# Optimization experiments

Measured on AMD Instinct MI355X. Metric: run time of the kernel, lower is better.

Reference implementation:

```python
import jax, jax.numpy as jnp
import numpy as np

N = 20000      # nodes
E = 320000     # edges (before self loops)
D_IN = 256
D_H = 256
D_E = 8
NEG_SLOPE = 0.2


def setup_inputs() -> dict:
    key = jax.random.key(0)
    ks = jax.random.split(key, 12)
    x = jax.random.normal(ks[0], (N, D_IN), jnp.float32)
    edge_index = jax.random.randint(ks[1], (2, E), 0, N, dtype=jnp.int32)
    edge_attr = jax.random.normal(ks[2], (E, D_E), jnp.float32)
    batch = jnp.zeros((N,), jnp.int32)

    def gat_params(k, d_in):
        k1, k2, k3 = jax.random.split(k, 3)
        W = jax.random.normal(k1, (d_in, D_H), jnp.float32) * (1.0 / np.sqrt(d_in))
        a_s = jax.random.normal(k2, (D_H,), jnp.float32) * 0.1
        a_d = jax.random.normal(k3, (D_H,), jnp.float32) * 0.1
        b = jnp.zeros((D_H,), jnp.float32)
        return W, a_s, a_d, b

    W1, as1, ad1, b1 = gat_params(ks[3], D_IN)
    W2, as2, ad2, b2 = gat_params(ks[4], D_H)
    W3, as3, ad3, b3 = gat_params(ks[5], D_H)
    return dict(x=x, edge_index=edge_index, edge_attr=edge_attr, batch=batch,
                W1=W1, as1=as1, ad1=ad1, b1=b1,
                W2=W2, as2=as2, ad2=ad2, b2=b2,
                W3=W3, as3=as3, ad3=ad3, b3=b3)


def gat_conv(x, src, dst, W, a_src, a_dst, b):
    # PyG GATConv, heads=1: h = x W; alpha_e = leakyrelu(<h_src,a_s> + <h_dst,a_d>)
    h = x @ W                                  # [N, D_H]
    s = h @ a_src                              # [N]
    d = h @ a_dst                              # [N]
    alpha = jax.nn.leaky_relu(s[src] + d[dst], NEG_SLOPE)   # [Etot]
    n = h.shape[0]
    m = jax.ops.segment_max(alpha, dst, num_segments=n)     # per-dst max
    ex = jnp.exp(alpha - m[dst])
    denom = jax.ops.segment_sum(ex, dst, num_segments=n)
    w = ex / (denom[dst] + 1e-16)
    out = jax.ops.segment_sum(h[src] * w[:, None], dst, num_segments=n)
    return out + b


def reference(x, edge_index, edge_attr, batch,
              W1, as1, ad1, b1, W2, as2, ad2, b2, W3, as3, ad3, b3):
    # row-normalize input features (zero norms -> 1e-8)
    norms = jnp.linalg.norm(x, axis=1, keepdims=True)
    norms = jnp.where(norms == 0, 1e-8, norms)
    x = x / norms

    # add self loops once (GATConv default add_self_loops=True);
    # edge_attr is ignored since edge_dim=None in GATConv defaults.
    loop = jnp.arange(N, dtype=edge_index.dtype)
    src = jnp.concatenate([edge_index[0], loop])
    dst = jnp.concatenate([edge_index[1], loop])

    x = jax.nn.gelu(gat_conv(x, src, dst, W1, as1, ad1, b1), approximate=False)
    x = jax.nn.gelu(gat_conv(x, src, dst, W2, as2, ad2, b2), approximate=False)
    x = jax.nn.gelu(gat_conv(x, src, dst, W3, as3, ad3, b3), approximate=False)
    return x
```

## Files before the change

kernel.cpp:

```cpp
#include <hip/hip_runtime.h>
#include <math.h>

#define NN 20000
#define EE 320000
#define DD 256
#define ETOT (EE + NN)
#define EDGE_CAP 1536

typedef __attribute__((ext_vector_type(8))) short bf8;
typedef __attribute__((ext_vector_type(4))) float f32x4;

__device__ __forceinline__ float gelu_exact(float x) {
    return 0.5f * x * (1.0f + erff(x * 0.70710678118654752f));
}

__device__ __forceinline__ unsigned short f2bf(float v) {
    unsigned u = __float_as_uint(v);
    u += 0x7fffu + ((u >> 16) & 1u);
    return (unsigned short)(u >> 16);
}
__device__ __forceinline__ float bf2f(unsigned short h) {
    return __uint_as_float(((unsigned)h) << 16);
}
__device__ __forceinline__ void split2(float v, unsigned short& hi, unsigned short& lo) {
    hi = f2bf(v);
    lo = f2bf(v - bf2f(hi));
}

__global__ __launch_bounds__(256) void norm_k(const float* __restrict__ X,
                                              unsigned short* __restrict__ Xh,
                                              unsigned short* __restrict__ Xl,
                                              float* __restrict__ sdZero,
                                              int* __restrict__ deg) {
    int t = threadIdx.x;
    int bid = blockIdx.x;
    if (t < 24) sdZero[bid * 24 + t] = 0.0f;
    if (t >= 32 && t < 36) deg[bid * 4 + (t - 32)] = 1;

    int wave = (bid * 256 + t) >> 6;
    int lane = t & 63;
    const float4 v = *(const float4*)&X[wave * DD + lane * 4];
    float ss = v.x * v.x + v.y * v.y + v.z * v.z + v.w * v.w;
    for (int off = 32; off > 0; off >>= 1) ss += __shfl_down(ss, off, 64);
    ss = __shfl(ss, 0, 64);
    float n = sqrtf(ss);
    if (n == 0.0f) n = 1e-8f;
    float inv = 1.0f / n;
    float o[4] = {v.x * inv, v.y * inv, v.z * inv, v.w * inv};
    ushort4 hv, lv;
    split2(o[0], hv.x, lv.x);
    split2(o[1], hv.y, lv.y);
    split2(o[2], hv.z, lv.z);
    split2(o[3], hv.w, lv.w);
    *(ushort4*)&Xh[wave * DD + lane * 4] = hv;
    *(ushort4*)&Xl[wave * DD + lane * 4] = lv;
}

__global__ __launch_bounds__(256) void splitw_k(const float* __restrict__ W1, const float* __restrict__ W2,
                                                const float* __restrict__ W3, unsigned short* __restrict__ Whl) {
    __shared__ float tile[64][65];
    int t = threadIdx.x;
    int k0 = blockIdx.x * 64;
    int c0 = blockIdx.y * 64;
    int z = blockIdx.z;
    const float* W = (z == 0) ? W1 : (z == 1) ? W2 : W3;
    unsigned short* Wht = Whl + (size_t)z * 2 * DD * DD;
    unsigned short* Wlt = Wht + DD * DD;
#pragma unroll
    for (int i = 0; i < 16; ++i) {
        int idx = t + i * 256;
        int r = idx >> 6, c = idx & 63;
        tile[r][c] = W[(k0 + r) * DD + c0 + c];
    }
    __syncthreads();
#pragma unroll
    for (int i = 0; i < 16; ++i) {
        int idx = t + i * 256;
        int r = idx >> 6, c = idx & 63;
        float v = tile[c][r];
        unsigned short hi, lo;
        split2(v, hi, lo);
        Wht[(c0 + r) * DD + k0 + c] = hi;
        Wlt[(c0 + r) * DD + k0 + c] = lo;
    }
}

__global__ void count_k(const int* __restrict__ ei, int* deg) {
    int e = blockIdx.x * 256 + threadIdx.x;
    if (e < EE) atomicAdd(&deg[ei[EE + e]], 1);
}

#define SCAN_T 1024
#define ITEMS 20
__global__ __launch_bounds__(SCAN_T) void scan_k(const int* __restrict__ deg, int* __restrict__ offs,
                                                 int* __restrict__ cursor, int* __restrict__ csr) {
    __shared__ int part[SCAN_T];
    int t = threadIdx.x;
    int base = t * ITEMS;
    int local[ITEMS];
    int sum = 0;
#pragma unroll
    for (int i = 0; i < ITEMS; ++i) {
        int idx = base + i;
        int v = (idx < NN) ? deg[idx] : 0;
        local[i] = v;
        sum += v;
    }
    part[t] = sum;
    __syncthreads();
    for (int s = 1; s < SCAN_T; s <<= 1) {
        int v = (t >= s) ? part[t - s] : 0;
        __syncthreads();
        part[t] += v;
        __syncthreads();
    }
    int run = (t == 0) ? 0 : part[t - 1];
#pragma unroll
    for (int i = 0; i < ITEMS; ++i) {
        int idx = base + i;
        if (idx < NN) {
            offs[idx] = run;
            cursor[idx] = run + 1;
            csr[run] = idx;
            run += local[i];
        }
    }
    if (t == SCAN_T - 1) offs[NN] = part[SCAN_T - 1];
}

__global__ void fill_k(const int* __restrict__ ei, int* cursor, int* __restrict__ csr) {
    int e = blockIdx.x * 256 + threadIdx.x;
    if (e < EE) {
        int s = ei[e];
        int d = ei[EE + e];
        int p = atomicAdd(&cursor[d], 1);
        csr[p] = s;
    }
}

#define LDB 40
__global__ __launch_bounds__(256) void gemm_sd(const unsigned short* __restrict__ Xh,
                                               const unsigned short* __restrict__ Xl,
                                               const unsigned short* __restrict__ Bh,
                                               const unsigned short* __restrict__ Bl,
                                               const float* __restrict__ a_s,
                                               const float* __restrict__ a_d,
                                               float* __restrict__ H,
                                               float* __restrict__ sArr,
                                               float* __restrict__ dArr) {
    __shared__ unsigned short sBh[128 * LDB], sBl[128 * LDB];
    int t = threadIdx.x;
    int m0 = blockIdx.x * 64;
    int n0 = blockIdx.y * 128;
    int w = t >> 6, l = t & 63;
    int rofs = l & 15, kch = l >> 4;

    f32x4 acc[8] = {};

    int c1 = t, c2 = t + 256;
    int br1 = c1 >> 2, bo1 = (c1 & 3) * 8;
    int br2 = c2 >> 2, bo2 = (c2 & 3) * 8;
    const unsigned short* Bh1 = &Bh[(n0 + br1) * DD + bo1];
    const unsigned short* Bh2 = &Bh[(n0 + br2) * DD + bo2];
    const unsigned short* Bl1 = &Bl[(n0 + br1) * DD + bo1];
    const unsigned short* Bl2 = &Bl[(n0 + br2) * DD + bo2];
    bf8 rbh1 = *(const bf8*)Bh1;
    bf8 rbh2 = *(const bf8*)Bh2;
    bf8 rbl1 = *(const bf8*)Bl1;
    bf8 rbl2 = *(const bf8*)Bl2;

    int arow = m0 + w * 16 + rofs;
    bool aval = arow < NN;
    const unsigned short* Ahp = &Xh[(size_t)arow * DD + kch * 8];
    const unsigned short* Alp = &Xl[(size_t)arow * DD + kch * 8];
    bf8 zero = {0, 0, 0, 0, 0, 0, 0, 0};
    bf8 ah = aval ? *(const bf8*)Ahp : zero;
    bf8 al = aval ? *(const bf8*)Alp : zero;

    for (int k0 = 0; k0 < DD; k0 += 32) {
        if (k0) __syncthreads();
        *(bf8*)&sBh[br1 * LDB + bo1] = rbh1;
        *(bf8*)&sBh[br2 * LDB + bo2] = rbh2;
        *(bf8*)&sBl[br1 * LDB + bo1] = rbl1;
        *(bf8*)&sBl[br2 * LDB + bo2] = rbl2;
        __syncthreads();
        int kn = k0 + 32;
        bf8 nah = zero, nal = zero;
        if (kn < DD) {
            rbh1 = *(const bf8*)(Bh1 + kn);
            rbh2 = *(const bf8*)(Bh2 + kn);
            rbl1 = *(const bf8*)(Bl1 + kn);
            rbl2 = *(const bf8*)(Bl2 + kn);
            if (aval) {
                nah = *(const bf8*)(Ahp + kn);
                nal = *(const bf8*)(Alp + kn);
            }
        }
#pragma unroll
        for (int nt = 0; nt < 8; ++nt) {
            int r = nt * 16 + rofs;
            bf8 bh = *(const bf8*)&sBh[r * LDB + kch * 8];
            bf8 bl = *(const bf8*)&sBl[r * LDB + kch * 8];
            acc[nt] = __builtin_amdgcn_mfma_f32_16x16x32_bf16(ah, bh, acc[nt], 0, 0, 0);
            acc[nt] = __builtin_amdgcn_mfma_f32_16x16x32_bf16(ah, bl, acc[nt], 0, 0, 0);
            acc[nt] = __builtin_amdgcn_mfma_f32_16x16x32_bf16(al, bh, acc[nt], 0, 0, 0);
        }
        ah = nah;
        al = nal;
    }
    int row0 = m0 + w * 16 + (l >> 4) * 4;
    int colb = l & 15;
    float sp[4] = {0, 0, 0, 0}, dp[4] = {0, 0, 0, 0};
#pragma unroll
    for (int nt = 0; nt < 8; ++nt) {
        int cc = n0 + nt * 16 + colb;
        float vas = a_s[cc], vad = a_d[cc];
#pragma unroll
        for (int r = 0; r < 4; ++r) {
            int row = row0 + r;
            if (row < NN) H[(size_t)row * DD + cc] = acc[nt][r];
            sp[r] += acc[nt][r] * vas;
            dp[r] += acc[nt][r] * vad;
        }
    }
#pragma unroll
    for (int m = 1; m < 16; m <<= 1) {
#pragma unroll
        for (int r = 0; r < 4; ++r) {
            sp[r] += __shfl_xor(sp[r], m, 64);
            dp[r] += __shfl_xor(dp[r], m, 64);
        }
    }
    if (colb == 0) {
#pragma unroll
        for (int r = 0; r < 4; ++r) {
            int row = row0 + r;
            if (row < NN) {
                atomicAdd(&sArr[row], sp[r]);
                atomicAdd(&dArr[row], dp[r]);
            }
        }
    }
}

__global__ __launch_bounds__(256) void spmm_k(const float* __restrict__ H, const float* __restrict__ sArr,
                                              const float* __restrict__ dArr, const int* __restrict__ offs,
                                              const int* __restrict__ csr, const float* __restrict__ bias,
                                              unsigned short* __restrict__ Oh,
                                              unsigned short* __restrict__ Ol,
                                              float* __restrict__ outf32) {
    __shared__ float wLds[EDGE_CAP];
    __shared__ int sLds[EDGE_CAP];
    int t = threadIdx.x;
    int sub = t & 7;
    int g = t >> 3;
    int dst0 = blockIdx.y * 32;
    int dst = dst0 + g;
    int dim = blockIdx.x * 32 + sub * 4;

    int blkBeg = offs[dst0];
    int beg = offs[dst], end = offs[dst + 1];
    float dd = dArr[dst];

    float den = 0.0f;
    for (int e = beg + sub; e < end; e += 8) {
        int s = csr[e];
        float a = sArr[s] + dd;
        a = (a > 0.0f) ? a : 0.2f * a;
        float wv = expf(a);
        wLds[e - blkBeg] = wv;
        sLds[e - blkBeg] = s;
        den += wv;
    }
    den += __shfl_xor(den, 1, 64);
    den += __shfl_xor(den, 2, 64);
    den += __shfl_xor(den, 4, 64);
    float inv = 1.0f / den;
    for (int e = beg + sub; e < end; e += 8) wLds[e - blkBeg] *= inv;
    __syncthreads();

    const float* Hs = H + dim;
    float4 A0 = make_float4(0, 0, 0, 0), A1 = A0, A2 = A0, A3 = A0;
    int e = beg - blkBeg, lend = end - blkBeg;
    for (; e + 3 < lend; e += 4) {
        int s0 = sLds[e], s1 = sLds[e + 1], s2 = sLds[e + 2], s3 = sLds[e + 3];
        float w0 = wLds[e], w1 = wLds[e + 1], w2 = wLds[e + 2], w3 = wLds[e + 3];
        const float4 h0 = *(const float4*)&Hs[(size_t)s0 * DD];
        const float4 h1 = *(const float4*)&Hs[(size_t)s1 * DD];
        const float4 h2 = *(const float4*)&Hs[(size_t)s2 * DD];
        const float4 h3 = *(const float4*)&Hs[(size_t)s3 * DD];
        A0.x += w0 * h0.x; A0.y += w0 * h0.y; A0.z += w0 * h0.z; A0.w += w0 * h0.w;
        A1.x += w1 * h1.x; A1.y += w1 * h1.y; A1.z += w1 * h1.z; A1.w += w1 * h1.w;
        A2.x += w2 * h2.x; A2.y += w2 * h2.y; A2.z += w2 * h2.z; A2.w += w2 * h2.w;
        A3.x += w3 * h3.x; A3.y += w3 * h3.y; A3.z += w3 * h3.z; A3.w += w3 * h3.w;
    }
    for (; e < lend; ++e) {
        int s0 = sLds[e];
        float w0 = wLds[e];
        const float4 h0 = *(const float4*)&Hs[(size_t)s0 * DD];
        A0.x += w0 * h0.x; A0.y += w0 * h0.y; A0.z += w0 * h0.z; A0.w += w0 * h0.w;
    }

    const float4 b = *(const float4*)&bias[dim];
    float o0 = gelu_exact(A0.x + A1.x + A2.x + A3.x + b.x);
    float o1 = gelu_exact(A0.y + A1.y + A2.y + A3.y + b.y);
    float o2 = gelu_exact(A0.z + A1.z + A2.z + A3.z + b.z);
    float o3 = gelu_exact(A0.w + A1.w + A2.w + A3.w + b.w);

    ushort4 hv, lv;
    split2(o0, hv.x, lv.x);
    split2(o1, hv.y, lv.y);
    split2(o2, hv.z, lv.z);
    split2(o3, hv.w, lv.w);
    *(ushort4*)&Oh[dst * DD + dim] = hv;
    *(ushort4*)&Ol[dst * DD + dim] = lv;
    if (outf32) {
        float4 o = make_float4(o0, o1, o2, o3);
        *(float4*)&outf32[dst * DD + dim] = o;
    }
}

extern "C" void kernel_launch(void* const* d_in, const int* in_sizes, int n_in,
                              void* d_out, int out_size, void* d_ws, size_t ws_size,
                              hipStream_t stream) {
    const float* x  = (const float*)d_in[0];
    const int* ei   = (const int*)d_in[1];
    const float* W1 = (const float*)d_in[4];
    const float* as1 = (const float*)d_in[5];
    const float* ad1 = (const float*)d_in[6];
    const float* b1 = (const float*)d_in[7];
    const float* W2 = (const float*)d_in[8];
    const float* as2 = (const float*)d_in[9];
    const float* ad2 = (const float*)d_in[10];
    const float* b2 = (const float*)d_in[11];
    const float* W3 = (const float*)d_in[12];
    const float* as3 = (const float*)d_in[13];
    const float* ad3 = (const float*)d_in[14];
    const float* b3 = (const float*)d_in[15];

    float* H = (float*)d_ws;
    unsigned short* Xh = (unsigned short*)(H + (size_t)NN * DD);
    unsigned short* Xl = Xh + (size_t)NN * DD;
    unsigned short* Whl = Xl + (size_t)NN * DD;
    float* sd = (float*)(Whl + (size_t)6 * DD * DD);
    int* offs = (int*)(sd + (size_t)6 * NN);
    int* cursor = offs + (NN + 1);
    int* csr = cursor + NN;
    int* deg = csr + ETOT;

    float* sA1 = sd,           *dA1 = sd + NN;
    float* sA2 = sd + 2 * NN,  *dA2 = sd + 3 * NN;
    float* sA3 = sd + 4 * NN,  *dA3 = sd + 5 * NN;
    unsigned short* Wt1 = Whl;
    unsigned short* Wt2 = Whl + (size_t)2 * DD * DD;
    unsigned short* Wt3 = Whl + (size_t)4 * DD * DD;

    norm_k<<<NN / 4, 256, 0, stream>>>(x, Xh, Xl, sd, deg);
    count_k<<<(EE + 255) / 256, 256, 0, stream>>>(ei, deg);
    scan_k<<<1, SCAN_T, 0, stream>>>(deg, offs, cursor, csr);
    fill_k<<<(EE + 255) / 256, 256, 0, stream>>>(ei, cursor, csr);
    splitw_k<<<dim3(4, 4, 3), 256, 0, stream>>>(W1, W2, W3, Whl);

    dim3 ggrid((NN + 63) / 64, DD / 128);
    dim3 sgrid(DD / 32, NN / 32);

    gemm_sd<<<ggrid, 256, 0, stream>>>(Xh, Xl, Wt1, Wt1 + DD * DD, as1, ad1, H, sA1, dA1);
    spmm_k<<<sgrid, 256, 0, stream>>>(H, sA1, dA1, offs, csr, b1, Xh, Xl, nullptr);
    gemm_sd<<<ggrid, 256, 0, stream>>>(Xh, Xl, Wt2, Wt2 + DD * DD, as2, ad2, H, sA2, dA2);
    spmm_k<<<sgrid, 256, 0, stream>>>(H, sA2, dA2, offs, csr, b2, Xh, Xl, nullptr);
    gemm_sd<<<ggrid, 256, 0, stream>>>(Xh, Xl, Wt3, Wt3 + DD * DD, as3, ad3, H, sA3, dA3);
    spmm_k<<<sgrid, 256, 0, stream>>>(H, sA3, dA3, offs, csr, b3, Xh, Xl, (float*)d_out);
}
```

Before: 337.1 us.

## Precompute edge attention weights once per layer and grid-stride SpMM blocks

Adds a separate alpha_k kernel that computes exp(leakyrelu) edge weights once per edge, using a new per-edge destination array written during CSR construction. Previously each of the 8 dim-column blocks recomputed them. The SpMM kernel now loads weights and source indices with vectorized copies into LDS, folds the normalization into the final scale, and grid-strides over destination groups with a fixed 313-row grid. The cost is an extra kernel launch and extra global traffic for the weight and destination arrays. EDGE_CAP grows slightly to allow for the aligned base.

```diff
diff --git a/kernel.cpp b/kernel.cpp
--- a/kernel.cpp
+++ b/kernel.cpp
@@ -5,7 +5,7 @@
 #define EE 320000
 #define DD 256
 #define ETOT (EE + NN)
-#define EDGE_CAP 1536
+#define EDGE_CAP 1544
 
 typedef __attribute__((ext_vector_type(8))) short bf8;
 typedef __attribute__((ext_vector_type(4))) float f32x4;
@@ -93,7 +93,8 @@
 #define SCAN_T 1024
 #define ITEMS 20
 __global__ __launch_bounds__(SCAN_T) void scan_k(const int* __restrict__ deg, int* __restrict__ offs,
-                                                 int* __restrict__ cursor, int* __restrict__ csr) {
+                                                 int* __restrict__ cursor, int* __restrict__ csr,
+                                                 int* __restrict__ csrD) {
     __shared__ int part[SCAN_T];
     int t = threadIdx.x;
     int base = t * ITEMS;
@@ -122,19 +123,35 @@
             offs[idx] = run;
             cursor[idx] = run + 1;
             csr[run] = idx;
+            csrD[run] = idx;
             run += local[i];
         }
     }
     if (t == SCAN_T - 1) offs[NN] = part[SCAN_T - 1];
 }
 
-__global__ void fill_k(const int* __restrict__ ei, int* cursor, int* __restrict__ csr) {
+__global__ void fill_k(const int* __restrict__ ei, int* cursor, int* __restrict__ csr,
+                       int* __restrict__ csrD) {
     int e = blockIdx.x * 256 + threadIdx.x;
     if (e < EE) {
         int s = ei[e];
         int d = ei[EE + e];
         int p = atomicAdd(&cursor[d], 1);
         csr[p] = s;
+        csrD[p] = d;
+    }
+}
+
+__global__ __launch_bounds__(256) void alpha_k(const float* __restrict__ sArr,
+                                               const float* __restrict__ dArr,
+                                               const int* __restrict__ csr,
+                                               const int* __restrict__ csrD,
+                                               float* __restrict__ wArr) {
+    int p = blockIdx.x * 256 + threadIdx.x;
+    if (p < ETOT) {
+        float a = sArr[csr[p]] + dArr[csrD[p]];
+        a = (a > 0.0f) ? a : 0.2f * a;
+        wArr[p] = expf(a);
     }
 }
 
@@ -243,9 +260,11 @@
     }
 }
 
-__global__ __launch_bounds__(256) void spmm_k(const float* __restrict__ H, const float* __restrict__ sArr,
-                                              const float* __restrict__ dArr, const int* __restrict__ offs,
-                                              const int* __restrict__ csr, const float* __restrict__ bias,
+__global__ __launch_bounds__(256) void spmm_k(const float* __restrict__ H,
+                                              const int* __restrict__ offs,
+                                              const int* __restrict__ csr,
+                                              const float* __restrict__ wArr,
+                                              const float* __restrict__ bias,
                                               unsigned short* __restrict__ Oh,
                                               unsigned short* __restrict__ Ol,
                                               float* __restrict__ outf32) {
@@ -254,69 +273,69 @@
     int t = threadIdx.x;
     int sub = t & 7;
     int g = t >> 3;
-    int dst0 = blockIdx.y * 32;
-    int dst = dst0 + g;
     int dim = blockIdx.x * 32 + sub * 4;
-
-    int blkBeg = offs[dst0];
-    int beg = offs[dst], end = offs[dst + 1];
-    float dd = dArr[dst];
-
-    float den = 0.0f;
-    for (int e = beg + sub; e < end; e += 8) {
-        int s = csr[e];
-        float a = sArr[s] + dd;
-        a = (a > 0.0f) ? a : 0.2f * a;
-        float wv = expf(a);
-        wLds[e - blkBeg] = wv;
-        sLds[e - blkBeg] = s;
-        den += wv;
-    }
-    den += __shfl_xor(den, 1, 64);
-    den += __shfl_xor(den, 2, 64);
-    den += __shfl_xor(den, 4, 64);
-    float inv = 1.0f / den;
-    for (int e = beg + sub; e < end; e += 8) wLds[e - blkBeg] *= inv;
-    __syncthreads();
-
     const float* Hs = H + dim;
-    float4 A0 = make_float4(0, 0, 0, 0), A1 = A0, A2 = A0, A3 = A0;
-    int e = beg - blkBeg, lend = end - blkBeg;
-    for (; e + 3 < lend; e += 4) {
-        int s0 = sLds[e], s1 = sLds[e + 1], s2 = sLds[e + 2], s3 = sLds[e + 3];
-        float w0 = wLds[e], w1 = wLds[e + 1], w2 = wLds[e + 2], w3 = wLds[e + 3];
-        const float4 h0 = *(const float4*)&Hs[(size_t)s0 * DD];
-        const float4 h1 = *(const float4*)&Hs[(size_t)s1 * DD];
-        const float4 h2 = *(const float4*)&Hs[(size_t)s2 * DD];
-        const float4 h3 = *(const float4*)&Hs[(size_t)s3 * DD];
-        A0.x += w0 * h0.x; A0.y += w0 * h0.y; A0.z += w0 * h0.z; A0.w += w0 * h0.w;
-        A1.x += w1 * h1.x; A1.y += w1 * h1.y; A1.z += w1 * h1.z; A1.w += w1 * h1.w;
-        A2.x += w2 * h2.x; A2.y += w2 * h2.y; A2.z += w2 * h2.z; A2.w += w2 * h2.w;
-        A3.x += w3 * h3.x; A3.y += w3 * h3.y; A3.z += w3 * h3.z; A3.w += w3 * h3.w;
-    }
-    for (; e < lend; ++e) {
-        int s0 = sLds[e];
-        float w0 = wLds[e];
-        const float4 h0 = *(const float4*)&Hs[(size_t)s0 * DD];
-        A0.x += w0 * h0.x; A0.y += w0 * h0.y; A0.z += w0 * h0.z; A0.w += w0 * h0.w;
-    }
-
-    const float4 b = *(const float4*)&bias[dim];
-    float o0 = gelu_exact(A0.x + A1.x + A2.x + A3.x + b.x);
-    float o1 = gelu_exact(A0.y + A1.y + A2.y + A3.y + b.y);
-    float o2 = gelu_exact(A0.z + A1.z + A2.z + A3.z + b.z);
-    float o3 = gelu_exact(A0.w + A1.w + A2.w + A3.w + b.w);
-
-    ushort4 hv, lv;
-    split2(o0, hv.x, lv.x);
-    split2(o1, hv.y, lv.y);
-    split2(o2, hv.z, lv.z);
-    split2(o3, hv.w, lv.w);
-    *(ushort4*)&Oh[dst * DD + dim] = hv;
-    *(ushort4*)&Ol[dst * DD + dim] = lv;
-    if (outf32) {
-        float4 o = make_float4(o0, o1, o2, o3);
-        *(float4*)&outf32[dst * DD + dim] = o;
+    const float4 bvec = *(const float4*)&bias[dim];
+
+    for (int grp = blockIdx.y; grp < NN / 32; grp += (int)gridDim.y) {
+        if (grp != (int)blockIdx.y) __syncthreads();
+        int dst0 = grp * 32;
+        int dst = dst0 + g;
+        int blkBeg = offs[dst0];
+        int blkEnd = offs[dst0 + 32];
+        int base = blkBeg & ~3;
+        int cnt = blkEnd - base;
+        for (int i = t * 4; i < cnt; i += 1024) {
+            *(float4*)&wLds[i] = *(const float4*)&wArr[base + i];
+            *(int4*)&sLds[i] = *(const int4*)&csr[base + i];
+        }
+        int beg = offs[dst], end = offs[dst + 1];
+        __syncthreads();
+
+        float den = 0.0f;
+        for (int e = beg + sub; e < end; e += 8) den += wLds[e - base];
+        den += __shfl_xor(den, 1, 64);
+        den += __shfl_xor(den, 2, 64);
+        den += __shfl_xor(den, 4, 64);
+        float inv = 1.0f / den;
+
+        float4 A0 = make_float4(0, 0, 0, 0), A1 = A0, A2 = A0, A3 = A0;
+        int e = beg - base, lend = end - base;
+        for (; e + 3 < lend; e += 4) {
+            int s0 = sLds[e], s1 = sLds[e + 1], s2 = sLds[e + 2], s3 = sLds[e + 3];
+            float w0 = wLds[e], w1 = wLds[e + 1], w2 = wLds[e + 2], w3 = wLds[e + 3];
+            const float4 h0 = *(const float4*)&Hs[(size_t)s0 * DD];
+            const float4 h1 = *(const float4*)&Hs[(size_t)s1 * DD];
+            const float4 h2 = *(const float4*)&Hs[(size_t)s2 * DD];
+            const float4 h3 = *(const float4*)&Hs[(size_t)s3 * DD];
+            A0.x += w0 * h0.x; A0.y += w0 * h0.y; A0.z += w0 * h0.z; A0.w += w0 * h0.w;
+            A1.x += w1 * h1.x; A1.y += w1 * h1.y; A1.z += w1 * h1.z; A1.w += w1 * h1.w;
+            A2.x += w2 * h2.x; A2.y += w2 * h2.y; A2.z += w2 * h2.z; A2.w += w2 * h2.w;
+            A3.x += w3 * h3.x; A3.y += w3 * h3.y; A3.z += w3 * h3.z; A3.w += w3 * h3.w;
+        }
+        for (; e < lend; ++e) {
+            int s0 = sLds[e];
+            float w0 = wLds[e];
+            const float4 h0 = *(const float4*)&Hs[(size_t)s0 * DD];
+            A0.x += w0 * h0.x; A0.y += w0 * h0.y; A0.z += w0 * h0.z; A0.w += w0 * h0.w;
+        }
+
+        float o0 = gelu_exact((A0.x + A1.x + A2.x + A3.x) * inv + bvec.x);
+        float o1 = gelu_exact((A0.y + A1.y + A2.y + A3.y) * inv + bvec.y);
+        float o2 = gelu_exact((A0.z + A1.z + A2.z + A3.z) * inv + bvec.z);
+        float o3 = gelu_exact((A0.w + A1.w + A2.w + A3.w) * inv + bvec.w);
+
+        ushort4 hv, lv;
+        split2(o0, hv.x, lv.x);
+        split2(o1, hv.y, lv.y);
+        split2(o2, hv.z, lv.z);
+        split2(o3, hv.w, lv.w);
+        *(ushort4*)&Oh[dst * DD + dim] = hv;
+        *(ushort4*)&Ol[dst * DD + dim] = lv;
+        if (outf32) {
+            float4 o = make_float4(o0, o1, o2, o3);
+            *(float4*)&outf32[dst * DD + dim] = o;
+        }
     }
 }
 
@@ -347,6 +366,8 @@
     int* cursor = offs + (NN + 1);
     int* csr = cursor + NN;
     int* deg = csr + ETOT;
+    int* csrD = deg + NN;
+    float* wArr = (float*)(csrD + ETOT);
 
     float* sA1 = sd,           *dA1 = sd + NN;
     float* sA2 = sd + 2 * NN,  *dA2 = sd + 3 * NN;
@@ -357,17 +378,21 @@
 
     norm_k<<<NN / 4, 256, 0, stream>>>(x, Xh, Xl, sd, deg);
     count_k<<<(EE + 255) / 256, 256, 0, stream>>>(ei, deg);
-    scan_k<<<1, SCAN_T, 0, stream>>>(deg, offs, cursor, csr);
-    fill_k<<<(EE + 255) / 256, 256, 0, stream>>>(ei, cursor, csr);
+    scan_k<<<1, SCAN_T, 0, stream>>>(deg, offs, cursor, csr, csrD);
+    fill_k<<<(EE + 255) / 256, 256, 0, stream>>>(ei, cursor, csr, csrD);
     splitw_k<<<dim3(4, 4, 3), 256, 0, stream>>>(W1, W2, W3, Whl);
 
     dim3 ggrid((NN + 63) / 64, DD / 128);
-    dim3 sgrid(DD / 32, NN / 32);
+    dim3 sgrid(DD / 32, 313);
+    int agrid = (ETOT + 255) / 256;
 
     gemm_sd<<<ggrid, 256, 0, stream>>>(Xh, Xl, Wt1, Wt1 + DD * DD, as1, ad1, H, sA1, dA1);
-    spmm_k<<<sgrid, 256, 0, stream>>>(H, sA1, dA1, offs, csr, b1, Xh, Xl, nullptr);
+    alpha_k<<<agrid, 256, 0, stream>>>(sA1, dA1, csr, csrD, wArr);
+    spmm_k<<<sgrid, 256, 0, stream>>>(H, offs, csr, wArr, b1, Xh, Xl, nullptr);
     gemm_sd<<<ggrid, 256, 0, stream>>>(Xh, Xl, Wt2, Wt2 + DD * DD, as2, ad2, H, sA2, dA2);
-    spmm_k<<<sgrid, 256, 0, stream>>>(H, sA2, dA2, offs, csr, b2, Xh, Xl, nullptr);
+    alpha_k<<<agrid, 256, 0, stream>>>(sA2, dA2, csr, csrD, wArr);
+    spmm_k<<<sgrid, 256, 0, stream>>>(H, offs, csr, wArr, b2, Xh, Xl, nullptr);
     gemm_sd<<<ggrid, 256, 0, stream>>>(Xh, Xl, Wt3, Wt3 + DD * DD, as3, ad3, H, sA3, dA3);
-    spmm_k<<<sgrid, 256, 0, stream>>>(H, sA3, dA3, offs, csr, b3, Xh, Xl, (float*)d_out);
-}
+    alpha_k<<<agrid, 256, 0, stream>>>(sA3, dA3, csr, csrD, wArr);
+    spmm_k<<<sgrid, 256, 0, stream>>>(H, offs, csr, wArr, b3, Xh, Xl, (float*)d_out);
+}
```

New measurement: 346.9 us. 2.9% more time.
